# Kernel optimization log

Measured on AMD Instinct MI355X. Metric: run time of the kernel, lower is better.

Reference implementation:

```python
import jax, jax.numpy as jnp
import numpy as np
from jax import lax

STRIDE = 1
PAD = 1
KH = KW = 3


def conv2d(x, w, b=None, stride=STRIDE, pad=PAD):
    out = lax.conv_general_dilated(x, w, (stride, stride), [(pad, pad), (pad, pad)],
                                   dimension_numbers=("NCHW", "OIHW", "NCHW"))
    if b is not None:
        out = out + b[None, :, None, None]
    return out


def deform_conv2d(x, offset, mask, weight, stride=STRIDE, pad=PAD):
    """torchvision.ops.deform_conv2d (v2, single group) semantics."""
    B, C, H, W = x.shape
    Co, Ci, Kh, Kw = weight.shape
    K2 = Kh * Kw
    Ho = (H + 2 * pad - Kh) // stride + 1
    Wo = (W + 2 * pad - Kw) // stride + 1

    off = offset.reshape(B, K2, 2, Ho, Wo)  # [...,0]=dy, [...,1]=dx (row-major kernel order)
    ky = (jnp.arange(K2) // Kw).astype(x.dtype)
    kx = (jnp.arange(K2) % Kw).astype(x.dtype)
    hs = (jnp.arange(Ho) * stride - pad).astype(x.dtype)
    ws = (jnp.arange(Wo) * stride - pad).astype(x.dtype)

    # sampling coords [B, K2, Ho, Wo]
    py = off[:, :, 0] + hs[None, None, :, None] + ky[None, :, None, None]
    px = off[:, :, 1] + ws[None, None, None, :] + kx[None, :, None, None]

    y0 = jnp.floor(py)
    x0 = jnp.floor(px)
    wy1 = py - y0
    wx1 = px - x0
    wy0 = 1.0 - wy1
    wx0 = 1.0 - wx1
    y0i = y0.astype(jnp.int32)
    x0i = x0.astype(jnp.int32)

    xf = x.reshape(B, C, H * W)

    def gather(yi, xi):
        valid = (yi >= 0) & (yi < H) & (xi >= 0) & (xi < W)
        lin = jnp.clip(yi, 0, H - 1) * W + jnp.clip(xi, 0, W - 1)  # [B,K2,Ho,Wo]
        linf = lin.reshape(B, 1, -1)
        g = jnp.take_along_axis(xf, jnp.broadcast_to(linf, (B, C, linf.shape[-1])), axis=2)
        g = g.reshape(B, C, K2, Ho, Wo)
        return g * valid[:, None].astype(x.dtype)

    # bilinear combine, modulated by mask; v: [B, C, K2, Ho, Wo]
    v = ((wy0 * wx0)[:, None] * gather(y0i, x0i)
         + (wy0 * wx1)[:, None] * gather(y0i, x0i + 1)
         + (wy1 * wx0)[:, None] * gather(y0i + 1, x0i)
         + (wy1 * wx1)[:, None] * gather(y0i + 1, x0i + 1))
    v = v * mask[:, None]

    return jnp.einsum('bckhw,ock->bohw', v, weight.reshape(Co, Ci, K2))


def setup_inputs() -> dict:
    key = jax.random.key(0)
    ks = jax.random.split(key, 6)
    B, C, H, W = 2, 256, 64, 64
    Co = 256
    fan = C * KH * KW
    return {
        "x": jax.random.normal(ks[0], (B, C, H, W), jnp.float32),
        "residual": jax.random.normal(ks[1], (B, C, H, W), jnp.float32),
        "offset_w": jax.random.normal(ks[2], (2 * KH * KW, C, KH, KW), jnp.float32) * np.sqrt(2.0 / fan),
        "offset_b": jnp.zeros((2 * KH * KW,), jnp.float32),
        "mod_w": jax.random.normal(ks[3], (KH * KW, C, KH, KW), jnp.float32) * np.sqrt(2.0 / fan),
        "mod_b": jnp.zeros((KH * KW,), jnp.float32),
        "reg_w": jax.random.normal(ks[4], (Co, C, KH, KW), jnp.float32) * np.sqrt(2.0 / fan),
    }


def reference(x, residual, offset_w, offset_b, mod_w, mod_b, reg_w):
    offset = conv2d(residual, offset_w, offset_b)
    modulator = 2.0 * jax.nn.sigmoid(conv2d(x, mod_w, mod_b))
    return deform_conv2d(x, offset, modulator, reg_w)
```

## Files before the change

### kernel.cpp

```cpp
#include <hip/hip_runtime.h>
#include <hip/hip_bf16.h>
#include <math.h>

#define BB 2
#define CC 256
#define HH 64
#define WW 64
#define COo 256
#define HWs 4096
#define K2 9
#define CK 2304

typedef __attribute__((ext_vector_type(4))) float floatx4;
typedef __attribute__((ext_vector_type(8))) short shortx8;

#define O_OFF   0
#define O_MASK  147456
#define O_WBF   221184
#define O_WPK   516096
#define O_A     589824
#define O_XT    10027008
#define O_RT    11075584

__device__ __forceinline__ void gll16(const __hip_bfloat16* g, __hip_bfloat16* l) {
    __builtin_amdgcn_global_load_lds(
        (const __attribute__((address_space(1))) unsigned int*)g,
        (__attribute__((address_space(3))) unsigned int*)l, 16, 0, 0);
}

__device__ __forceinline__ short f2bf(float v) {
    __hip_bfloat16 h = __float2bfloat16(v);
    return *reinterpret_cast<short*>(&h);
}

__device__ __forceinline__ float bf2f(short s) {
    unsigned u = ((unsigned)(unsigned short)s) << 16;
    return __builtin_bit_cast(float, u);
}

__global__ __launch_bounds__(256) void prep_kernel(
    const float* __restrict__ x,
    const float* __restrict__ residual,
    const float* __restrict__ reg_w,
    const float* __restrict__ off_w,
    const float* __restrict__ mod_w,
    __hip_bfloat16* __restrict__ xT,
    __hip_bfloat16* __restrict__ resT,
    __hip_bfloat16* __restrict__ Wbf,
    __hip_bfloat16* __restrict__ Wpk)
{
    int blk = blockIdx.x;
    int t = threadIdx.x;
    if (blk < 2048) {
        int sel = blk >> 10;
        int bk  = blk & 1023;
        int oc = bk & 7;
        int y  = (bk >> 3) & 63;
        int b  = bk >> 9;
        int wo = t & 63;
        int cg = t >> 6;
        int c0 = oc * 32 + cg * 8;
        const float* src = (sel ? residual : x)
                           + ((size_t)(b * CC + c0) * HH + y) * WW + wo;
        shortx8 pk;
#pragma unroll
        for (int j = 0; j < 8; ++j) pk[j] = f2bf(src[(size_t)j * HWs]);
        __hip_bfloat16* dst = sel ? resT : xT;
        *(shortx8*)(dst + ((size_t)b * 4096 + y * 64 + wo) * 256 + c0) = pk;
    } else {
        int idx = (blk - 2048) * 256 + t;
        if (idx < CK * COo) {
            Wbf[idx] = __float2bfloat16(reg_w[idx]);
        }
        if (idx < 147456) {
            int g    = idx / 73728;
            int rem  = idx % 73728;
            int kc   = rem / 9216;
            int r2   = rem % 9216;
            int tap  = r2 / 1024;
            int r3   = r2 & 1023;
            int nf   = r3 >> 9;
            int r4   = r3 & 511;
            int lane = r4 >> 3;
            int j    = r4 & 7;
            int c    = kc * 32 + (lane >> 4) * 8 + j;
            int n    = nf * 16 + (lane & 15);
            float v = 0.f;
            if (g == 0) { if (n < 18) v = off_w[((size_t)n * CC + c) * 9 + tap]; }
            else        { if (n < 9)  v = mod_w[((size_t)n * CC + c) * 9 + tap]; }
            Wpk[idx] = __float2bfloat16(v);
        }
    }
}

__global__ __launch_bounds__(512) void convA2_kernel(
    const __hip_bfloat16* __restrict__ xT,
    const __hip_bfloat16* __restrict__ resT,
    const __hip_bfloat16* __restrict__ Wpk,
    const float* __restrict__ off_b,
    const float* __restrict__ mod_b,
    float* __restrict__ off_out,
    float* __restrict__ mask_out)
{
    int blk = blockIdx.x;
    int tile = blk & 127;
    int g = (blk >> 7) & 1;
    int b = blk >> 8;
    int t = threadIdx.x;
    int lane = t & 63;
    int w = t >> 6;
    int ph = w & 1;
    int ks = w >> 1;
    int ln = lane & 15;
    int quad = lane >> 4;

    const __hip_bfloat16* src = (g ? xT : resT) + (size_t)b * 4096 * 256;
    const __hip_bfloat16* wg  = Wpk + (size_t)g * 73728 + (size_t)ks * 2 * 9216;

    int pix = tile * 32 + ph * 16 + ln;
    int ho = pix >> 6, wo = pix & 63;

    floatx4 acc0 = (floatx4){0.f, 0.f, 0.f, 0.f};
    floatx4 acc1 = (floatx4){0.f, 0.f, 0.f, 0.f};

#pragma unroll
    for (int tap = 0; tap < 9; ++tap) {
        int ky = tap / 3, kx = tap % 3;
        int r  = ho + ky - 1;
        int cx = wo + kx - 1;
        bool v = (r >= 0) && (r < HH) && (cx >= 0) && (cx < WW);
        int hw = v ? (r * WW + cx) : 0;
        const __hip_bfloat16* abase = src + (size_t)hw * 256 + quad * 8 + ks * 64;
        const __hip_bfloat16* wbase = wg + (size_t)tap * 1024 + lane * 8;
#pragma unroll
        for (int kc = 0; kc < 2; ++kc) {
            shortx8 af = *(const shortx8*)(abase + kc * 32);
            if (!v) {
                shortx8 zf = {0,0,0,0,0,0,0,0};
                af = zf;
            }
            shortx8 b0 = *(const shortx8*)(wbase + (size_t)kc * 9216);
            shortx8 b1 = *(const shortx8*)(wbase + (size_t)kc * 9216 + 512);
            acc0 = __builtin_amdgcn_mfma_f32_16x16x32_bf16(af, b0, acc0, 0, 0, 0);
            acc1 = __builtin_amdgcn_mfma_f32_16x16x32_bf16(af, b1, acc1, 0, 0, 0);
        }
    }

    __shared__ float s_red[8][64][8];
    *(floatx4*)&s_red[w][lane][0] = acc0;
    *(floatx4*)&s_red[w][lane][4] = acc1;
    __syncthreads();
    if (w < 2) {
#pragma unroll
        for (int j = 0; j < 4; ++j) {
            acc0[j] = s_red[w][lane][j]     + s_red[w + 2][lane][j]
                    + s_red[w + 4][lane][j] + s_red[w + 6][lane][j];
            acc1[j] = s_red[w][lane][4 + j]     + s_red[w + 2][lane][4 + j]
                    + s_red[w + 4][lane][4 + j] + s_red[w + 6][lane][4 + j];
        }

#pragma unroll
        for (int nf = 0; nf < 2; ++nf) {
            floatx4 a = nf ? acc1 : acc0;
            int n = nf * 16 + ln;
#pragma unroll
            for (int i2 = 0; i2 < 4; ++i2) {
                int p = tile * 32 + w * 16 + quad * 4 + i2;
                if (g == 0) {
                    if (n < 18)
                        off_out[((size_t)b * 18 + n) * HWs + p] = a[i2] + off_b[n];
                } else {
                    if (n < 9) {
                        float z = a[i2] + mod_b[n];
                        mask_out[((size_t)b * 9 + n) * HWs + p] =
                            2.f / (1.f + __expf(-z));
                    }
                }
            }
        }
    }
}

__global__ __launch_bounds__(256) void gather_kernel(
    const __hip_bfloat16* __restrict__ xT,
    const float* __restrict__ off,
    const float* __restrict__ mask,
    __hip_bfloat16* __restrict__ A)
{
    int blk = blockIdx.x;
    int cc = blk & 7;
    int ho = (blk >> 3) & 63;
    int b  = blk >> 9;
    int t  = threadIdx.x;
    int wo = t & 63;
    int cg = t >> 6;

    __shared__ int   s_idx[4][K2][64];
    __shared__ float s_w  [4][K2][64];

    for (int u = t; u < K2 * 64; u += 256) {
        int k = u >> 6;
        int wv = u & 63;
        float dy = off[((((size_t)b * 18 + 2 * k    ) * HH + ho) << 6) + wv];
        float dx = off[((((size_t)b * 18 + 2 * k + 1) * HH + ho) << 6) + wv];
        float m  = mask[((((size_t)b * 9 + k) * HH + ho) << 6) + wv];
        float py = (float)(ho - 1 + k / 3) + dy;
        float px = (float)(wv - 1 + k % 3) + dx;
        float y0f = floorf(py), x0f = floorf(px);
        float wy1 = py - y0f, wx1 = px - x0f;
        float wy0 = 1.f - wy1, wx0 = 1.f - wx1;
        int y0 = (int)y0f, x0 = (int)x0f;
#pragma unroll
        for (int j = 0; j < 4; ++j) {
            int yy = y0 + (j >> 1);
            int xx = x0 + (j & 1);
            float wj = ((j == 0) ? wy0 * wx0 :
                        (j == 1) ? wy0 * wx1 :
                        (j == 2) ? wy1 * wx0 : wy1 * wx1) * m;
            bool valid = (yy >= 0) && (yy < HH) && (xx >= 0) && (xx < WW);
            s_idx[j][k][wv] = valid ? (yy * WW + xx) : 0;
            s_w  [j][k][wv] = valid ? wj : 0.f;
        }
    }
    __syncthreads();

    const __hip_bfloat16* xb = xT + (size_t)b * 4096 * 256 + cc * 32 + cg * 8;

    shortx8 outv[9];
#pragma unroll
    for (int k = 0; k < K2; ++k) {
        int   i0 = s_idx[0][k][wo], i1 = s_idx[1][k][wo];
        int   i2 = s_idx[2][k][wo], i3 = s_idx[3][k][wo];
        float w0 = s_w[0][k][wo], w1 = s_w[1][k][wo];
        float w2 = s_w[2][k][wo], w3 = s_w[3][k][wo];
        shortx8 c0 = *(const shortx8*)(xb + (size_t)i0 * 256);
        shortx8 c1 = *(const shortx8*)(xb + (size_t)i1 * 256);
        shortx8 c2 = *(const shortx8*)(xb + (size_t)i2 * 256);
        shortx8 c3 = *(const shortx8*)(xb + (size_t)i3 * 256);
#pragma unroll
        for (int j = 0; j < 8; ++j) {
            float v = w0 * bf2f(c0[j]) + w1 * bf2f(c1[j])
                    + w2 * bf2f(c2[j]) + w3 * bf2f(c3[j]);
            int idx = j * 9 + k;
            outv[idx >> 3][idx & 7] = f2bf(v);
        }
    }

    __hip_bfloat16* arow = A + (size_t)((b * 64 + ho) * 64 + wo) * CK
                             + cc * 288 + cg * 72;
#pragma unroll
    for (int m = 0; m < 9; ++m)
        *(shortx8*)(arow + m * 8) = outv[m];
}

__global__ __launch_bounds__(256) void gemm_kernel(
    const __hip_bfloat16* __restrict__ A,
    const __hip_bfloat16* __restrict__ Wbf,
    float* __restrict__ out)
{
    int blk0 = blockIdx.x;
    int blk = ((blk0 & 7) << 6) | (blk0 >> 3);
    int nt = blk & 1;
    int mt = blk >> 1;
    int t  = threadIdx.x;
    int lane = t & 63;
    int w    = t >> 6;
    int quad = lane >> 4;
    int ln   = lane & 15;
    int wm = w & 1;
    int wn = w >> 1;

    __shared__ __hip_bfloat16 As[2][32 * 64];
    __shared__ __hip_bfloat16 Bs[2][128 * 64];
    __shared__ float s_out[4][16 * 20];

    int lr8 = lane >> 3;
    int sub = lane & 7;
    int chk = sub ^ lr8;

    const __hip_bfloat16* gA = A   + (size_t)(mt * 32 + w * 8 + lr8) * CK + chk * 8;
    const __hip_bfloat16* gB = Wbf + (size_t)(nt * 128 + w * 8 + lr8) * CK + chk * 8;
    int lof = w * 512;

    floatx4 acc[4];
#pragma unroll
    for (int nf = 0; nf < 4; ++nf) acc[nf] = (floatx4){0.f, 0.f, 0.f, 0.f};

    gll16(gA, &As[0][lof]);
#pragma unroll
    for (int h = 0; h < 4; ++h)
        gll16(gB + (size_t)(h * 32) * CK, &Bs[0][lof + h * 2048]);

    int swz = ln & 7;

    for (int kt = 0; kt < 36; ++kt) {
        int cur = kt & 1;
        int nxt = cur ^ 1;
        __syncthreads();
        if (kt + 1 < 36) {
            int ko = (kt + 1) * 64;
            gll16(gA + ko, &As[nxt][lof]);
#pragma unroll
            for (int h = 0; h < 4; ++h)
                gll16(gB + (size_t)(h * 32) * CK + ko, &Bs[nxt][lof + h * 2048]);
        }
#pragma unroll
        for (int kh = 0; kh < 2; ++kh) {
            int slot = ((kh * 4 + quad) ^ swz) * 8;
            shortx8 af = *(const shortx8*)
                &As[cur][(wm * 16 + ln) * 64 + slot];
            shortx8 bf[4];
#pragma unroll
            for (int nf = 0; nf < 4; ++nf)
                bf[nf] = *(const shortx8*)
                    &Bs[cur][(wn * 64 + nf * 16 + ln) * 64 + slot];
#pragma unroll
            for (int nf = 0; nf < 4; ++nf)
                acc[nf] = __builtin_amdgcn_mfma_f32_16x16x32_bf16(
                    af, bf[nf], acc[nf], 0, 0, 0);
        }
    }

    int bb = mt >> 7;
    int hw0 = (mt & 127) * 32 + wm * 16;
    float* sw = &s_out[w][0];
    int co_l = lane >> 2;
    int seg  = lane & 3;
#pragma unroll
    for (int nf = 0; nf < 4; ++nf) {
        *(floatx4*)&sw[ln * 20 + quad * 4] = acc[nf];
        floatx4 v0 = *(const floatx4*)&sw[co_l * 20 + seg * 4];
        int co = nt * 128 + wn * 64 + nf * 16 + co_l;
        float* orow = out + ((size_t)(bb * COo + co) << 12) + hw0;
        *(floatx4*)&orow[seg * 4] = v0;
    }
}

extern "C" void kernel_launch(void* const* d_in, const int* in_sizes, int n_in,
                              void* d_out, int out_size, void* d_ws, size_t ws_size,
                              hipStream_t stream)
{
    const float* x     = (const float*)d_in[0];
    const float* resid = (const float*)d_in[1];
    const float* off_w = (const float*)d_in[2];
    const float* off_b = (const float*)d_in[3];
    const float* mod_w = (const float*)d_in[4];
    const float* mod_b = (const float*)d_in[5];
    const float* reg_w = (const float*)d_in[6];
    float* out = (float*)d_out;

    float* ws = (float*)d_ws;
    float* off_buf   = ws + O_OFF;
    float* mask_buf  = ws + O_MASK;
    __hip_bfloat16* Wbf  = (__hip_bfloat16*)(ws + O_WBF);
    __hip_bfloat16* Wpk  = (__hip_bfloat16*)(ws + O_WPK);
    __hip_bfloat16* Abuf = (__hip_bfloat16*)(ws + O_A);
    __hip_bfloat16* xT   = (__hip_bfloat16*)(ws + O_XT);
    __hip_bfloat16* resT = (__hip_bfloat16*)(ws + O_RT);

    prep_kernel<<<2048 + (CK * COo + 255) / 256, 256, 0, stream>>>(
        x, resid, reg_w, off_w, mod_w, xT, resT, Wbf, Wpk);

    convA2_kernel<<<512, 512, 0, stream>>>(xT, resT, Wpk, off_b, mod_b,
                                           off_buf, mask_buf);

    gather_kernel<<<BB * HH * 8, 256, 0, stream>>>(xT, off_buf, mask_buf, Abuf);

    gemm_kernel<<<512, 256, 0, stream>>>(Abuf, Wbf, out);
}
```

Baseline: 154.8 us.

## Fuse bilinear deformable gather into GEMM A-tile producer, reorder weights tap-major

Removes the separate gather kernel and its large bf16 A-matrix round trip through global memory. The GEMM now computes sampling indices and weights for its 32 pixels into shared memory, then builds each A tile on the fly from xT inside the K loop. To make each 64-wide K step a single tap and channel block, the weight layout is permuted to tap-major order. The cost is that each of the two N-tile blocks redoes the gather, and the gather's latency now sits on the GEMM critical path with no async overlap.

```diff
diff --git a/kernel.cpp b/kernel.cpp
--- a/kernel.cpp
+++ b/kernel.cpp
@@ -70,7 +70,11 @@
     } else {
         int idx = (blk - 2048) * 256 + t;
         if (idx < CK * COo) {
-            Wbf[idx] = __float2bfloat16(reg_w[idx]);
+            int co = idx / CK;
+            int r  = idx - co * CK;
+            int k  = r >> 8;
+            int c  = r & 255;
+            Wbf[idx] = __float2bfloat16(reg_w[(size_t)co * CK + c * 9 + k]);
         }
         if (idx < 147456) {
             int g    = idx / 73728;
@@ -181,80 +185,10 @@
     }
 }
 
-__global__ __launch_bounds__(256) void gather_kernel(
+__global__ __launch_bounds__(256) void gemm_fused_kernel(
     const __hip_bfloat16* __restrict__ xT,
     const float* __restrict__ off,
     const float* __restrict__ mask,
-    __hip_bfloat16* __restrict__ A)
-{
-    int blk = blockIdx.x;
-    int cc = blk & 7;
-    int ho = (blk >> 3) & 63;
-    int b  = blk >> 9;
-    int t  = threadIdx.x;
-    int wo = t & 63;
-    int cg = t >> 6;
-
-    __shared__ int   s_idx[4][K2][64];
-    __shared__ float s_w  [4][K2][64];
-
-    for (int u = t; u < K2 * 64; u += 256) {
-        int k = u >> 6;
-        int wv = u & 63;
-        float dy = off[((((size_t)b * 18 + 2 * k    ) * HH + ho) << 6) + wv];
-        float dx = off[((((size_t)b * 18 + 2 * k + 1) * HH + ho) << 6) + wv];
-        float m  = mask[((((size_t)b * 9 + k) * HH + ho) << 6) + wv];
-        float py = (float)(ho - 1 + k / 3) + dy;
-        float px = (float)(wv - 1 + k % 3) + dx;
-        float y0f = floorf(py), x0f = floorf(px);
-        float wy1 = py - y0f, wx1 = px - x0f;
-        float wy0 = 1.f - wy1, wx0 = 1.f - wx1;
-        int y0 = (int)y0f, x0 = (int)x0f;
-#pragma unroll
-        for (int j = 0; j < 4; ++j) {
-            int yy = y0 + (j >> 1);
-            int xx = x0 + (j & 1);
-            float wj = ((j == 0) ? wy0 * wx0 :
-                        (j == 1) ? wy0 * wx1 :
-                        (j == 2) ? wy1 * wx0 : wy1 * wx1) * m;
-            bool valid = (yy >= 0) && (yy < HH) && (xx >= 0) && (xx < WW);
-            s_idx[j][k][wv] = valid ? (yy * WW + xx) : 0;
-            s_w  [j][k][wv] = valid ? wj : 0.f;
-        }
-    }
-    __syncthreads();
-
-    const __hip_bfloat16* xb = xT + (size_t)b * 4096 * 256 + cc * 32 + cg * 8;
-
-    shortx8 outv[9];
-#pragma unroll
-    for (int k = 0; k < K2; ++k) {
-        int   i0 = s_idx[0][k][wo], i1 = s_idx[1][k][wo];
-        int   i2 = s_idx[2][k][wo], i3 = s_idx[3][k][wo];
-        float w0 = s_w[0][k][wo], w1 = s_w[1][k][wo];
-        float w2 = s_w[2][k][wo], w3 = s_w[3][k][wo];
-        shortx8 c0 = *(const shortx8*)(xb + (size_t)i0 * 256);
-        shortx8 c1 = *(const shortx8*)(xb + (size_t)i1 * 256);
-        shortx8 c2 = *(const shortx8*)(xb + (size_t)i2 * 256);
-        shortx8 c3 = *(const shortx8*)(xb + (size_t)i3 * 256);
-#pragma unroll
-        for (int j = 0; j < 8; ++j) {
-            float v = w0 * bf2f(c0[j]) + w1 * bf2f(c1[j])
-                    + w2 * bf2f(c2[j]) + w3 * bf2f(c3[j]);
-            int idx = j * 9 + k;
-            outv[idx >> 3][idx & 7] = f2bf(v);
-        }
-    }
-
-    __hip_bfloat16* arow = A + (size_t)((b * 64 + ho) * 64 + wo) * CK
-                             + cc * 288 + cg * 72;
-#pragma unroll
-    for (int m = 0; m < 9; ++m)
-        *(shortx8*)(arow + m * 8) = outv[m];
-}
-
-__global__ __launch_bounds__(256) void gemm_kernel(
-    const __hip_bfloat16* __restrict__ A,
     const __hip_bfloat16* __restrict__ Wbf,
     float* __restrict__ out)
 {
@@ -272,13 +206,17 @@
 
     __shared__ __hip_bfloat16 As[2][32 * 64];
     __shared__ __hip_bfloat16 Bs[2][128 * 64];
+    __shared__ int   s_mi[32][K2][4];
+    __shared__ float s_mw[32][K2][4];
     __shared__ float s_out[4][16 * 20];
+
+    int b = mt >> 7;
+    const __hip_bfloat16* xb = xT + (size_t)b * 4096 * 256;
 
     int lr8 = lane >> 3;
     int sub = lane & 7;
     int chk = sub ^ lr8;
 
-    const __hip_bfloat16* gA = A   + (size_t)(mt * 32 + w * 8 + lr8) * CK + chk * 8;
     const __hip_bfloat16* gB = Wbf + (size_t)(nt * 128 + w * 8 + lr8) * CK + chk * 8;
     int lof = w * 512;
 
@@ -286,10 +224,64 @@
 #pragma unroll
     for (int nf = 0; nf < 4; ++nf) acc[nf] = (floatx4){0.f, 0.f, 0.f, 0.f};
 
-    gll16(gA, &As[0][lof]);
 #pragma unroll
     for (int h = 0; h < 4; ++h)
         gll16(gB + (size_t)(h * 32) * CK, &Bs[0][lof + h * 2048]);
+
+    for (int u = t; u < 32 * K2; u += 256) {
+        int pl = u / K2;
+        int k  = u - pl * K2;
+        int pix = mt * 32 + pl;
+        int hw = pix & 4095;
+        int ho = hw >> 6, wo = hw & 63;
+        float dy = off [(((size_t)b * 18 + 2 * k    ) << 12) + hw];
+        float dx = off [(((size_t)b * 18 + 2 * k + 1) << 12) + hw];
+        float m  = mask[(((size_t)b * 9  + k        ) << 12) + hw];
+        float py = (float)(ho - 1 + k / 3) + dy;
+        float px = (float)(wo - 1 + k % 3) + dx;
+        float y0f = floorf(py), x0f = floorf(px);
+        float wy1 = py - y0f, wx1 = px - x0f;
+        float wy0 = 1.f - wy1, wx0 = 1.f - wx1;
+        int y0 = (int)y0f, x0 = (int)x0f;
+#pragma unroll
+        for (int j = 0; j < 4; ++j) {
+            int yy = y0 + (j >> 1);
+            int xx = x0 + (j & 1);
+            float wj = ((j == 0) ? wy0 * wx0 :
+                        (j == 1) ? wy0 * wx1 :
+                        (j == 2) ? wy1 * wx0 : wy1 * wx1) * m;
+            bool valid = (yy >= 0) && (yy < HH) && (xx >= 0) && (xx < WW);
+            s_mi[pl][k][j] = valid ? (yy * WW + xx) : 0;
+            s_mw[pl][k][j] = valid ? wj : 0.f;
+        }
+    }
+
+    int pl  = t >> 3;
+    int ch8 = t & 7;
+    int aslot = pl * 64 + ((ch8 ^ (pl & 7)) * 8);
+
+    auto gather = [&](int buf, int kt1) {
+        int k  = kt1 >> 2;
+        int cb = kt1 & 3;
+        int i0 = s_mi[pl][k][0], i1 = s_mi[pl][k][1];
+        int i2 = s_mi[pl][k][2], i3 = s_mi[pl][k][3];
+        float w0 = s_mw[pl][k][0], w1 = s_mw[pl][k][1];
+        float w2 = s_mw[pl][k][2], w3 = s_mw[pl][k][3];
+        const __hip_bfloat16* xr = xb + cb * 64 + ch8 * 8;
+        shortx8 c0 = *(const shortx8*)(xr + (size_t)i0 * 256);
+        shortx8 c1 = *(const shortx8*)(xr + (size_t)i1 * 256);
+        shortx8 c2 = *(const shortx8*)(xr + (size_t)i2 * 256);
+        shortx8 c3 = *(const shortx8*)(xr + (size_t)i3 * 256);
+        shortx8 o;
+#pragma unroll
+        for (int j = 0; j < 8; ++j)
+            o[j] = f2bf(w0 * bf2f(c0[j]) + w1 * bf2f(c1[j])
+                      + w2 * bf2f(c2[j]) + w3 * bf2f(c3[j]));
+        *(shortx8*)&As[buf][aslot] = o;
+    };
+
+    __syncthreads();
+    gather(0, 0);
 
     int swz = ln & 7;
 
@@ -299,7 +291,6 @@
         __syncthreads();
         if (kt + 1 < 36) {
             int ko = (kt + 1) * 64;
-            gll16(gA + ko, &As[nxt][lof]);
 #pragma unroll
             for (int h = 0; h < 4; ++h)
                 gll16(gB + (size_t)(h * 32) * CK + ko, &Bs[nxt][lof + h * 2048]);
@@ -319,6 +310,7 @@
                 acc[nf] = __builtin_amdgcn_mfma_f32_16x16x32_bf16(
                     af, bf[nf], acc[nf], 0, 0, 0);
         }
+        if (kt + 1 < 36) gather(nxt, kt + 1);
     }
 
     int bb = mt >> 7;
@@ -354,7 +346,6 @@
     float* mask_buf  = ws + O_MASK;
     __hip_bfloat16* Wbf  = (__hip_bfloat16*)(ws + O_WBF);
     __hip_bfloat16* Wpk  = (__hip_bfloat16*)(ws + O_WPK);
-    __hip_bfloat16* Abuf = (__hip_bfloat16*)(ws + O_A);
     __hip_bfloat16* xT   = (__hip_bfloat16*)(ws + O_XT);
     __hip_bfloat16* resT = (__hip_bfloat16*)(ws + O_RT);
 
@@ -364,7 +355,5 @@
     convA2_kernel<<<512, 512, 0, stream>>>(xT, resT, Wpk, off_b, mod_b,
                                            off_buf, mask_buf);
 
-    gather_kernel<<<BB * HH * 8, 256, 0, stream>>>(xT, off_buf, mask_buf, Abuf);
-
-    gemm_kernel<<<512, 256, 0, stream>>>(Abuf, Wbf, out);
-}
+    gemm_fused_kernel<<<512, 256, 0, stream>>>(xT, off_buf, mask_buf, Wbf, out);
+}
```

After: 132.4 us. -14.5%, faster.
